# Kernel optimization log

Measured on AMD Instinct MI355X. Metric: run time of the kernel, lower is better.

## Reference

```python
import jax, jax.numpy as jnp
import numpy as np

N, E = 50000, 800000
D_IN, D_HID, D_OUT = 256, 64, 32
LEAKY_SLOPE = 0.2  # PyG GATConv default negative_slope


def _gat(x, src, dst, W, a_src, a_dst, b, n):
    """Single-head PyG-style GATConv: gather -> edge softmax(dst) -> scatter."""
    h = x @ W                                            # [N, C]
    e = jax.nn.leaky_relu((h * a_src).sum(-1)[src] + (h * a_dst).sum(-1)[dst], LEAKY_SLOPE)  # [E]
    m = jax.ops.segment_max(e, dst, num_segments=n)      # per-dst max for stable softmax
    m = jnp.where(jnp.isfinite(m), m, 0.0)               # empty segments -> 0
    p = jnp.exp(e - m[dst])
    s = jax.ops.segment_sum(p, dst, num_segments=n)
    alpha = p / (s[dst] + 1e-16)                         # PyG softmax eps
    out = jax.ops.segment_sum(alpha[:, None] * h[src], dst, num_segments=n) + b
    return out, alpha


def setup_inputs() -> dict:
    key = jax.random.key(0)
    ks = jax.random.split(key, 16)
    g = lambda k, shape, sc: jax.random.normal(k, shape, jnp.float32) * sc
    glorot = lambda fi, fo: (2.0 / (fi + fo)) ** 0.5
    return {
        "x": g(ks[0], (N, D_IN), 1.0),
        "edge_index": jax.random.randint(ks[1], (2, E), 0, N),
        "W1": g(ks[2], (D_IN, D_HID), glorot(D_IN, D_HID)),
        "a1_src": g(ks[3], (D_HID,), 0.1),
        "a1_dst": g(ks[4], (D_HID,), 0.1),
        "b1": jnp.zeros((D_HID,), jnp.float32),
        "W2": g(ks[5], (D_HID, D_OUT), glorot(D_HID, D_OUT)),
        "a2_src": g(ks[6], (D_OUT,), 0.1),
        "a2_dst": g(ks[7], (D_OUT,), 0.1),
        "b2": jnp.zeros((D_OUT,), jnp.float32),
        "W3": g(ks[8], (D_HID, D_OUT), glorot(D_HID, D_OUT)),
        "a3_src": g(ks[9], (D_OUT,), 0.1),
        "a3_dst": g(ks[10], (D_OUT,), 0.1),
        "b3": jnp.zeros((D_OUT,), jnp.float32),
        "Wl": g(ks[11], (D_OUT, D_OUT), glorot(D_OUT, D_OUT)),
        "bl": jnp.zeros((D_OUT,), jnp.float32),
    }


def reference(x, edge_index, W1, a1_src, a1_dst, b1, W2, a2_src, a2_dst, b2,
              W3, a3_src, a3_dst, b3, Wl, bl):
    n = x.shape[0]
    src, dst = edge_index[0], edge_index[1]
    # eval mode: dropout(p=0.6) is identity
    h1, _ = _gat(x, src, dst, W1, a1_src, a1_dst, b1, n)
    h1 = jax.nn.elu(h1)
    mean, alpha = _gat(h1, src, dst, W2, a2_src, a2_dst, b2, n)
    mean = jax.nn.relu(mean)
    # conv_var uses PyG default add_self_loops=True
    loop = jnp.arange(n)
    src3 = jnp.concatenate([src, loop])
    dst3 = jnp.concatenate([dst, loop])
    var, _ = _gat(h1, src3, dst3, W3, a3_src, a3_dst, b3, n)
    mean = mean @ Wl + bl
    return mean, var, alpha
```

## Files before the change

kernel.cpp:

```cpp
#include <hip/hip_runtime.h>
#include <hip/hip_fp16.h>
#include <math.h>

#define N_NODES 50000
#define N_EDGES 800000
#define D_INF   256
#define D_HID   64
#define D_OUTF  32
#define LEAKY   0.2f

#define MT 32
#define KB 16

__device__ __forceinline__ float leaky_relu(float x){ return x >= 0.f ? x : LEAKY * x; }

union H4 { __half2 h[2]; float2 f; };
union H8 { __half2 h[4]; float4 f; };

__device__ __forceinline__ float ldg_f(const float* base, unsigned byteoff){
  return *(const float*)((const char*)base + byteoff);
}

__global__ void k_zero(int* __restrict__ deg){
  int i = blockIdx.x * blockDim.x + threadIdx.x;
  if (i < N_NODES) deg[i] = 0;
}

__global__ void k_deg(const int* __restrict__ dst, int* __restrict__ deg,
                      int* __restrict__ rank){
  int i = blockIdx.x * blockDim.x + threadIdx.x;
  if (i < N_EDGES) rank[i] = atomicAdd(&deg[dst[i]], 1);
}

__global__ __launch_bounds__(256) void k_scan_a(const int* __restrict__ deg, int* __restrict__ bsum){
  __shared__ int ws[4];
  int b = blockIdx.x, t = threadIdx.x, i = b * 256 + t;
  int x = (i < N_NODES) ? deg[i] : 0;
  #pragma unroll
  for (int off = 32; off; off >>= 1) x += __shfl_down(x, off, 64);
  if ((t & 63) == 0) ws[t >> 6] = x;
  __syncthreads();
  if (t == 0) bsum[b] = ws[0] + ws[1] + ws[2] + ws[3];
}

__global__ __launch_bounds__(256) void k_scan_b(int* __restrict__ bsum, int nb,
      const float* __restrict__ W2, const float* __restrict__ W3,
      const float* __restrict__ a2s, const float* __restrict__ a2d,
      const float* __restrict__ a3s, const float* __restrict__ a3d,
      float* __restrict__ prew){
  __shared__ int ws[4];
  int t = threadIdx.x, lane = t & 63, wv = t >> 6;
  int x = (t < nb) ? bsum[t] : 0;
  #pragma unroll
  for (int off = 1; off < 64; off <<= 1){
    int y = __shfl_up(x, off, 64);
    if (lane >= off) x += y;
  }
  if (lane == 63) ws[wv] = x;
  __syncthreads();
  int add = 0;
  for (int w = 0; w < wv; ++w) add += ws[w];
  x += add;
  if (t < nb) bsum[t] = x;

  int vec = t >> 6, k = t & 63;
  const float* W = (vec < 2) ? W2 : W3;
  const float* a = (vec == 0) ? a2s : (vec == 1) ? a2d : (vec == 2) ? a3s : a3d;
  float s = 0.f;
  #pragma unroll 8
  for (int c = 0; c < D_OUTF; ++c) s = fmaf(W[k * D_OUTF + c], a[c], s);
  prew[t] = s;
}

__global__ __launch_bounds__(256) void k_scan_c(const int* __restrict__ deg,
        const int* __restrict__ bsum, int* __restrict__ rowptr){
  __shared__ int ws[4];
  int b = blockIdx.x, t = threadIdx.x, i = b * 256 + t;
  int lane = t & 63, wv = t >> 6;
  int x = (i < N_NODES) ? deg[i] : 0;
  #pragma unroll
  for (int off = 1; off < 64; off <<= 1){
    int y = __shfl_up(x, off, 64);
    if (lane >= off) x += y;
  }
  if (lane == 63) ws[wv] = x;
  __syncthreads();
  int add = (b > 0) ? bsum[b - 1] : 0;
  for (int w = 0; w < wv; ++w) add += ws[w];
  x += add;
  if (i < N_NODES) rowptr[i + 1] = x;
  if (b == 0 && t == 0) rowptr[0] = 0;
}

__global__ void k_fill(const int* __restrict__ src, const int* __restrict__ dst,
                       const int* __restrict__ rowptr, const int* __restrict__ rank,
                       int* __restrict__ srcs){
  int i = blockIdx.x * blockDim.x + threadIdx.x;
  if (i < N_EDGES){
    srcs[rowptr[dst[i]] + rank[i]] = src[i];
  }
}

__global__ __launch_bounds__(256) void k_gemm1(const float* __restrict__ x,
        const float* __restrict__ W1,
        const float* __restrict__ a_src, const float* __restrict__ a_dst,
        __half* __restrict__ h1h, float* __restrict__ es, float* __restrict__ ed){
  __shared__ float xs[2][MT][KB + 4];
  __shared__ float ws[2][KB][D_HID];
  const int tid = threadIdx.x;
  const int tc  = tid & 15;
  const int tr  = tid >> 4;
  const int row0 = blockIdx.x * MT;

  const int lxr = tid >> 2;
  const int lxp = (tid & 3) << 2;
  const int gxrow = row0 + lxr;
  const bool xok = (tid < 128) && (gxrow < N_NODES);
  const float* xbase = x + (size_t)gxrow * D_INF + lxp;
  const int lwr = tid >> 4;
  const int lwp = (tid & 15) << 2;
  const float* wbase = W1 + lwr * D_HID + lwp;

  float4 xv = xok ? *(const float4*)xbase : make_float4(0.f,0.f,0.f,0.f);
  float4 wv = *(const float4*)wbase;
  if (tid < 128) *(float4*)&xs[0][lxr][lxp] = xv;
  *(float4*)&ws[0][lwr][lwp] = wv;
  __syncthreads();

  float acc[2][4] = {};
  int b = 0;
  #pragma unroll 1
  for (int ks = 0; ks < D_INF / KB; ++ks){
    if (ks < D_INF / KB - 1){
      xv = xok ? *(const float4*)(xbase + (ks + 1) * KB) : make_float4(0.f,0.f,0.f,0.f);
      wv = *(const float4*)(wbase + (size_t)(ks + 1) * KB * D_HID);
    }
    #pragma unroll
    for (int k4 = 0; k4 < KB / 4; ++k4){
      float4 xr4[2];
      #pragma unroll
      for (int r = 0; r < 2; ++r)
        xr4[r] = *(float4*)&xs[b][(tr << 1) + r][k4 << 2];
      #pragma unroll
      for (int j = 0; j < 4; ++j){
        float4 w4 = *(float4*)&ws[b][(k4 << 2) + j][tc << 2];
        #pragma unroll
        for (int r = 0; r < 2; ++r){
          float xk = (j == 0) ? xr4[r].x : (j == 1) ? xr4[r].y : (j == 2) ? xr4[r].z : xr4[r].w;
          acc[r][0] = fmaf(xk, w4.x, acc[r][0]);
          acc[r][1] = fmaf(xk, w4.y, acc[r][1]);
          acc[r][2] = fmaf(xk, w4.z, acc[r][2]);
          acc[r][3] = fmaf(xk, w4.w, acc[r][3]);
        }
      }
    }
    if (ks < D_INF / KB - 1){
      if (tid < 128) *(float4*)&xs[b ^ 1][lxr][lxp] = xv;
      *(float4*)&ws[b ^ 1][lwr][lwp] = wv;
    }
    __syncthreads();
    b ^= 1;
  }

  float as0 = a_src[tc << 2], as1 = a_src[(tc << 2) + 1],
        as2 = a_src[(tc << 2) + 2], as3 = a_src[(tc << 2) + 3];
  float ad0 = a_dst[tc << 2], ad1 = a_dst[(tc << 2) + 1],
        ad2 = a_dst[(tc << 2) + 2], ad3 = a_dst[(tc << 2) + 3];
  #pragma unroll
  for (int r = 0; r < 2; ++r){
    int row = row0 + (tr << 1) + r;
    float ps = acc[r][0]*as0 + acc[r][1]*as1 + acc[r][2]*as2 + acc[r][3]*as3;
    float pd = acc[r][0]*ad0 + acc[r][1]*ad1 + acc[r][2]*ad2 + acc[r][3]*ad3;
    #pragma unroll
    for (int off = 1; off < 16; off <<= 1){
      ps += __shfl_xor(ps, off, 64);
      pd += __shfl_xor(pd, off, 64);
    }
    if (row < N_NODES){
      H4 u;
      u.h[0] = __floats2half2_rn(acc[r][0], acc[r][1]);
      u.h[1] = __floats2half2_rn(acc[r][2], acc[r][3]);
      *(float2*)&h1h[(size_t)row * D_HID + (tc << 2)] = u.f;
      if (tc == 0){ es[row] = ps; ed[row] = pd; }
    }
  }
}

__global__ __launch_bounds__(256) void k_agg1(const int* __restrict__ rowptr,
      const int* __restrict__ srcs, const __half* __restrict__ h1,
      const float* __restrict__ es, const float* __restrict__ ed,
      const float* __restrict__ b1, __half* __restrict__ h1act){
  int t = threadIdx.x, lane = t & 63, wv = t >> 6;
  int nh = lane >> 5, sub = lane & 31;
  int slot2 = sub >> 3, cg = sub & 7;
  unsigned coff = cg << 4;

  int node = blockIdx.x * 8 + wv * 2 + nh;
  int beg = rowptr[node], end = rowptr[node + 1];
  int len = end - beg;
  int lenO = __shfl_xor(len, 32, 64);
  int lenmax = len > lenO ? len : lenO;
  int fallback = (len > 0) ? end - 1 : 0;
  float edv = ed[node];
  float4 aL = {0,0,0,0}, aH = {0,0,0,0};
  float ss = 0.f;
  for (int off = 0; off < lenmax; off += 16){
    int sA[4]; float4 vr[4]; float p[4];
    #pragma unroll
    for (int u = 0; u < 4; ++u){
      int idx = beg + off + (u << 2) + slot2;
      sA[u] = srcs[idx < end ? idx : fallback];
    }
    #pragma unroll
    for (int u = 0; u < 4; ++u)
      vr[u] = *(const float4*)((const char*)h1 + ((unsigned)sA[u] << 7) + coff);
    #pragma unroll
    for (int u = 0; u < 4; ++u){
      float e = __expf(leaky_relu(ldg_f(es, (unsigned)sA[u] << 2) + edv));
      p[u] = ((off + (u << 2) + slot2) < len) ? e : 0.f;
    }
    #pragma unroll
    for (int u = 0; u < 4; ++u){
      ss += p[u];
      H8 hh; hh.f = vr[u];
      float2 c0 = __half22float2(hh.h[0]);
      float2 c1 = __half22float2(hh.h[1]);
      float2 c2 = __half22float2(hh.h[2]);
      float2 c3 = __half22float2(hh.h[3]);
      aL.x = fmaf(p[u], c0.x, aL.x); aL.y = fmaf(p[u], c0.y, aL.y);
      aL.z = fmaf(p[u], c1.x, aL.z); aL.w = fmaf(p[u], c1.y, aL.w);
      aH.x = fmaf(p[u], c2.x, aH.x); aH.y = fmaf(p[u], c2.y, aH.y);
      aH.z = fmaf(p[u], c3.x, aH.z); aH.w = fmaf(p[u], c3.y, aH.w);
    }
  }
  #pragma unroll
  for (int off = 8; off <= 16; off <<= 1){
    aL.x += __shfl_xor(aL.x, off, 64); aL.y += __shfl_xor(aL.y, off, 64);
    aL.z += __shfl_xor(aL.z, off, 64); aL.w += __shfl_xor(aL.w, off, 64);
    aH.x += __shfl_xor(aH.x, off, 64); aH.y += __shfl_xor(aH.y, off, 64);
    aH.z += __shfl_xor(aH.z, off, 64); aH.w += __shfl_xor(aH.w, off, 64);
    ss   += __shfl_xor(ss,   off, 64);
  }
  if (slot2 == 0){
    float inv = 1.f / (ss + 1e-16f);
    int ch0 = cg << 3;
    float4 bA = *(const float4*)&b1[ch0];
    float4 bB = *(const float4*)&b1[ch0 + 4];
    float v0 = aL.x * inv + bA.x; v0 = v0 > 0.f ? v0 : expm1f(v0);
    float v1 = aL.y * inv + bA.y; v1 = v1 > 0.f ? v1 : expm1f(v1);
    float v2 = aL.z * inv + bA.z; v2 = v2 > 0.f ? v2 : expm1f(v2);
    float v3 = aL.w * inv + bA.w; v3 = v3 > 0.f ? v3 : expm1f(v3);
    float v4 = aH.x * inv + bB.x; v4 = v4 > 0.f ? v4 : expm1f(v4);
    float v5 = aH.y * inv + bB.y; v5 = v5 > 0.f ? v5 : expm1f(v5);
    float v6 = aH.z * inv + bB.z; v6 = v6 > 0.f ? v6 : expm1f(v6);
    float v7 = aH.w * inv + bB.w; v7 = v7 > 0.f ? v7 : expm1f(v7);
    H8 o;
    o.h[0] = __floats2half2_rn(v0, v1);
    o.h[1] = __floats2half2_rn(v2, v3);
    o.h[2] = __floats2half2_rn(v4, v5);
    o.h[3] = __floats2half2_rn(v6, v7);
    *(float4*)&h1act[(size_t)node * D_HID + ch0] = o.f;
  }
}

__global__ __launch_bounds__(256) void k_gemm23(const __half* __restrict__ h1acth,
        const float* __restrict__ W2, const float* __restrict__ W3,
        const float* __restrict__ prew,
        __half* __restrict__ h23h, float2* __restrict__ es23,
        float2* __restrict__ edinv2, float* __restrict__ ed3){
  __shared__ float hs[64][68];
  __shared__ float wsd[64][64];
  __shared__ float sprew[256];
  const int tid = threadIdx.x;
  const int row0 = blockIdx.x * 64;

  {
    int r = tid >> 2, cg = tid & 3;
    int grow = row0 + r;
    bool ok = grow < N_NODES;
    const float4* hrow = (const float4*)(h1acth + (size_t)grow * D_HID + cg * 16);
    H8 q0, q1;
    q0.f = ok ? hrow[0] : make_float4(0,0,0,0);
    q1.f = ok ? hrow[1] : make_float4(0,0,0,0);
    float* dsth = &hs[r][cg * 16];
    #pragma unroll
    for (int j = 0; j < 4; ++j){
      float2 f = __half22float2(q0.h[j]);
      dsth[j * 2] = f.x; dsth[j * 2 + 1] = f.y;
    }
    #pragma unroll
    for (int j = 0; j < 4; ++j){
      float2 f = __half22float2(q1.h[j]);
      dsth[8 + j * 2] = f.x; dsth[8 + j * 2 + 1] = f.y;
    }
    int k = tid >> 2;
    const float* Wsrc = (cg < 2) ? W2 : W3;
    int cbase = (cg & 1) * 16;
    float4* dstw = (float4*)&wsd[k][cg * 16];
    const float4* srcw = (const float4*)&Wsrc[k * D_OUTF + cbase];
    #pragma unroll
    for (int j = 0; j < 4; ++j) dstw[j] = srcw[j];
    sprew[tid] = prew[tid];
  }
  __syncthreads();

  {
    int r = tid >> 2, q = tid & 3, row = row0 + r;
    float d0 = 0.f, d1 = 0.f, d2 = 0.f, d3 = 0.f;
    #pragma unroll
    for (int k = 0; k < 16; ++k){
      float hval = hs[r][(q << 4) + k];
      d0 = fmaf(hval, sprew[(q << 4) + k], d0);
      d1 = fmaf(hval, sprew[64 + (q << 4) + k], d1);
      d2 = fmaf(hval, sprew[128 + (q << 4) + k], d2);
      d3 = fmaf(hval, sprew[192 + (q << 4) + k], d3);
    }
    #pragma unroll
    for (int off = 1; off < 4; off <<= 1){
      d0 += __shfl_xor(d0, off, 64);
      d1 += __shfl_xor(d1, off, 64);
      d2 += __shfl_xor(d2, off, 64);
      d3 += __shfl_xor(d3, off, 64);
    }
    if (q == 0 && row < N_NODES){
      es23[row] = make_float2(d0, d2);
      edinv2[row].x = d1;
      ed3[row] = d3;
    }
  }

  const int tc = tid & 15, tr = tid >> 4;
  float acc[4][4] = {};
  #pragma unroll
  for (int k4 = 0; k4 < 16; ++k4){
    float4 xr4[4];
    #pragma unroll
    for (int r = 0; r < 4; ++r)
      xr4[r] = *(float4*)&hs[(tr << 2) + r][k4 << 2];
    #pragma unroll
    for (int j = 0; j < 4; ++j){
      float4 w4 = *(float4*)&wsd[(k4 << 2) + j][tc << 2];
      #pragma unroll
      for (int r = 0; r < 4; ++r){
        float xk = (j == 0) ? xr4[r].x : (j == 1) ? xr4[r].y : (j == 2) ? xr4[r].z : xr4[r].w;
        acc[r][0] = fmaf(xk, w4.x, acc[r][0]);
        acc[r][1] = fmaf(xk, w4.y, acc[r][1]);
        acc[r][2] = fmaf(xk, w4.z, acc[r][2]);
        acc[r][3] = fmaf(xk, w4.w, acc[r][3]);
      }
    }
  }
  #pragma unroll
  for (int r = 0; r < 4; ++r){
    int row = row0 + (tr << 2) + r;
    if (row < N_NODES){
      H4 u;
      u.h[0] = __floats2half2_rn(acc[r][0], acc[r][1]);
      u.h[1] = __floats2half2_rn(acc[r][2], acc[r][3]);
      *(float2*)&h23h[(size_t)row * 64 + (tc << 2)] = u.f;
    }
  }
}

__global__ __launch_bounds__(256) void k_agg23(const int* __restrict__ rowptr,
   const int* __restrict__ srcs, const __half* __restrict__ h23,
   const float2* __restrict__ es23, float2* __restrict__ edinv2,
   const float* __restrict__ ed3,
   const float* __restrict__ b2, const float* __restrict__ b3,
   const float* __restrict__ Wlin, const float* __restrict__ blin,
   float* __restrict__ mean_out, float* __restrict__ var_out){
  __shared__ float sWl[D_OUTF * D_OUTF];
  int t = threadIdx.x, lane = t & 63, wv = t >> 6;
  int nh = lane >> 5, sub = lane & 31;
  int slot2 = sub >> 3, cg = sub & 7;
  int layer = cg >> 2;
  unsigned coff = cg << 4;
  for (int idx = t; idx < D_OUTF * D_OUTF; idx += 256) sWl[idx] = Wlin[idx];
  __syncthreads();

  int node = blockIdx.x * 8 + wv * 2 + nh;
  int beg = rowptr[node], end = rowptr[node + 1];
  int len = end - beg;
  int lenO = __shfl_xor(len, 32, 64);
  int lenmax = len > lenO ? len : lenO;
  int fallback = (len > 0) ? end - 1 : 0;
  float edv = layer ? ed3[node] : edinv2[node].x;
  float4 aL = {0,0,0,0}, aH = {0,0,0,0};
  float ss = 0.f;
  for (int off = 0; off < lenmax; off += 16){
    int sA[4]; float4 vr[4]; float p[4];
    #pragma unroll
    for (int u = 0; u < 4; ++u){
      int idx = beg + off + (u << 2) + slot2;
      sA[u] = srcs[idx < end ? idx : fallback];
    }
    #pragma unroll
    for (int u = 0; u < 4; ++u)
      vr[u] = *(const float4*)((const char*)h23 + ((unsigned)sA[u] << 7) + coff);
    #pragma unroll
    for (int u = 0; u < 4; ++u){
      float2 e2 = *(const float2*)((const char*)es23 + ((unsigned)sA[u] << 3));
      float esv = layer ? e2.y : e2.x;
      float e = __expf(leaky_relu(esv + edv));
      p[u] = ((off + (u << 2) + slot2) < len) ? e : 0.f;
    }
    #pragma unroll
    for (int u = 0; u < 4; ++u){
      ss += p[u];
      H8 hh; hh.f = vr[u];
      float2 c0 = __half22float2(hh.h[0]);
      float2 c1 = __half22float2(hh.h[1]);
      float2 c2 = __half22float2(hh.h[2]);
      float2 c3 = __half22float2(hh.h[3]);
      aL.x = fmaf(p[u], c0.x, aL.x); aL.y = fmaf(p[u], c0.y, aL.y);
      aL.z = fmaf(p[u], c1.x, aL.z); aL.w = fmaf(p[u], c1.y, aL.w);
      aH.x = fmaf(p[u], c2.x, aH.x); aH.y = fmaf(p[u], c2.y, aH.y);
      aH.z = fmaf(p[u], c3.x, aH.z); aH.w = fmaf(p[u], c3.y, aH.w);
    }
  }
  #pragma unroll
  for (int off = 8; off <= 16; off <<= 1){
    aL.x += __shfl_xor(aL.x, off, 64); aL.y += __shfl_xor(aL.y, off, 64);
    aL.z += __shfl_xor(aL.z, off, 64); aL.w += __shfl_xor(aL.w, off, 64);
    aH.x += __shfl_xor(aH.x, off, 64); aH.y += __shfl_xor(aH.y, off, 64);
    aH.z += __shfl_xor(aH.z, off, 64); aH.w += __shfl_xor(aH.w, off, 64);
    ss   += __shfl_xor(ss,   off, 64);
  }

  {
    float psr = __expf(leaky_relu(es23[node].y + ed3[node]));
    float psg = layer ? psr : 0.f;
    H8 hh; hh.f = *(const float4*)((const char*)h23 + ((unsigned)node << 7) + coff);
    float2 c0 = __half22float2(hh.h[0]);
    float2 c1 = __half22float2(hh.h[1]);
    float2 c2 = __half22float2(hh.h[2]);
    float2 c3 = __half22float2(hh.h[3]);
    aL.x = fmaf(psg, c0.x, aL.x); aL.y = fmaf(psg, c0.y, aL.y);
    aL.z = fmaf(psg, c1.x, aL.z); aL.w = fmaf(psg, c1.y, aL.w);
    aH.x = fmaf(psg, c2.x, aH.x); aH.y = fmaf(psg, c2.y, aH.y);
    aH.z = fmaf(psg, c3.x, aH.z); aH.w = fmaf(psg, c3.y, aH.w);
    ss += psg;
  }
  float inv = 1.f / (ss + 1e-16f);

  float m0=0,m1=0,m2=0,m3=0,m4=0,m5=0,m6=0,m7=0;
  if (!layer){
    int ch0 = cg << 3;
    float4 bA = *(const float4*)&b2[ch0];
    float4 bB = *(const float4*)&b2[ch0 + 4];
    m0 = aL.x * inv + bA.x; m0 = m0 > 0.f ? m0 : 0.f;
    m1 = aL.y * inv + bA.y; m1 = m1 > 0.f ? m1 : 0.f;
    m2 = aL.z * inv + bA.z; m2 = m2 > 0.f ? m2 : 0.f;
    m3 = aL.w * inv + bA.w; m3 = m3 > 0.f ? m3 : 0.f;
    m4 = aH.x * inv + bB.x; m4 = m4 > 0.f ? m4 : 0.f;
    m5 = aH.y * inv + bB.y; m5 = m5 > 0.f ? m5 : 0.f;
    m6 = aH.z * inv + bB.z; m6 = m6 > 0.f ? m6 : 0.f;
    m7 = aH.w * inv + bB.w; m7 = m7 > 0.f ? m7 : 0.f;
  } else if (slot2 == 0){
    int ch0 = (cg & 3) << 3;
    float4 bA = *(const float4*)&b3[ch0];
    float4 bB = *(const float4*)&b3[ch0 + 4];
    float4 oA = { aL.x * inv + bA.x, aL.y * inv + bA.y, aL.z * inv + bA.z, aL.w * inv + bA.w };
    float4 oB = { aH.x * inv + bB.x, aH.y * inv + bB.y, aH.z * inv + bB.z, aH.w * inv + bB.w };
    *(float4*)&var_out[(size_t)node * D_OUTF + ch0]     = oA;
    *(float4*)&var_out[(size_t)node * D_OUTF + ch0 + 4] = oB;
  }

  {
    int c = sub;
    int lbase = lane & 32;
    float o = blin[c];
    #pragma unroll
    for (int cgs = 0; cgs < 4; ++cgs){
      int sl = lbase | cgs;
      float q0 = __shfl(m0, sl, 64), q1 = __shfl(m1, sl, 64);
      float q2 = __shfl(m2, sl, 64), q3 = __shfl(m3, sl, 64);
      float q4 = __shfl(m4, sl, 64), q5 = __shfl(m5, sl, 64);
      float q6 = __shfl(m6, sl, 64), q7 = __shfl(m7, sl, 64);
      int j0 = cgs << 3;
      o = fmaf(q0, sWl[(j0+0) * D_OUTF + c], o);
      o = fmaf(q1, sWl[(j0+1) * D_OUTF + c], o);
      o = fmaf(q2, sWl[(j0+2) * D_OUTF + c], o);
      o = fmaf(q3, sWl[(j0+3) * D_OUTF + c], o);
      o = fmaf(q4, sWl[(j0+4) * D_OUTF + c], o);
      o = fmaf(q5, sWl[(j0+5) * D_OUTF + c], o);
      o = fmaf(q6, sWl[(j0+6) * D_OUTF + c], o);
      o = fmaf(q7, sWl[(j0+7) * D_OUTF + c], o);
    }
    mean_out[(size_t)node * D_OUTF + c] = o;
  }
  if (sub == 0) edinv2[node].y = inv;
}

__global__ __launch_bounds__(256) void k_alpha(const int* __restrict__ src,
    const int* __restrict__ dst,
    const float2* __restrict__ es23, const float2* __restrict__ edinv2,
    float* __restrict__ alpha_out){
  int e = blockIdx.x * blockDim.x + threadIdx.x;
  if (e < N_EDGES){
    int s = src[e], d = dst[e];
    float2 ei = *(const float2*)((const char*)edinv2 + ((unsigned)d << 3));
    float esv = ((const float2*)((const char*)es23 + ((unsigned)s << 3)))->x;
    alpha_out[e] = __expf(leaky_relu(esv + ei.x)) * ei.y;
  }
}

extern "C" void kernel_launch(void* const* d_in, const int* in_sizes, int n_in,
                              void* d_out, int out_size, void* d_ws, size_t ws_size,
                              hipStream_t stream) {
  const float* x   = (const float*)d_in[0];
  const int*   ei  = (const int*)d_in[1];
  const int*   src = ei;
  const int*   dst = ei + N_EDGES;
  const float* W1  = (const float*)d_in[2];
  const float* a1s = (const float*)d_in[3];
  const float* a1d = (const float*)d_in[4];
  const float* b1  = (const float*)d_in[5];
  const float* W2  = (const float*)d_in[6];
  const float* a2s = (const float*)d_in[7];
  const float* a2d = (const float*)d_in[8];
  const float* b2  = (const float*)d_in[9];
  const float* W3  = (const float*)d_in[10];
  const float* a3s = (const float*)d_in[11];
  const float* a3d = (const float*)d_in[12];
  const float* b3  = (const float*)d_in[13];
  const float* Wl  = (const float*)d_in[14];
  const float* bl  = (const float*)d_in[15];

  float* out       = (float*)d_out;
  float* mean_out  = out;
  float* var_out   = out + (size_t)N_NODES * D_OUTF;
  float* alpha_out = out + 2 * (size_t)N_NODES * D_OUTF;

  const int NSCAN = (N_NODES + 255) / 256;

  int* deg      = (int*)d_ws;
  int* rowptr   = deg + N_NODES;
  int* bsum     = rowptr + (N_NODES + 1);
  int* rank     = bsum + NSCAN;
  int* srcs     = rank + N_EDGES;
  size_t ioff   = (size_t)((srcs + N_EDGES) - (int*)d_ws);
  ioff = (ioff + 3) & ~(size_t)3;
  __half* h1    = (__half*)((int*)d_ws + ioff);
  __half* h1act = h1 + (size_t)N_NODES * 64;
  __half* h23   = h1act + (size_t)N_NODES * 64;
  float* es1    = (float*)(h23 + (size_t)N_NODES * 64);
  float* ed1    = es1 + N_NODES;
  float* ed3    = ed1 + N_NODES;
  float* prew   = ed3 + N_NODES;
  float2* es23  = (float2*)(prew + 256);
  float2* edinv2= es23 + N_NODES;

  k_zero  <<<NSCAN, 256, 0, stream>>>(deg);
  k_deg   <<<(N_EDGES + 255) / 256, 256, 0, stream>>>(dst, deg, rank);
  k_scan_a<<<NSCAN, 256, 0, stream>>>(deg, bsum);
  k_scan_b<<<1, 256, 0, stream>>>(bsum, NSCAN, W2, W3, a2s, a2d, a3s, a3d, prew);
  k_scan_c<<<NSCAN, 256, 0, stream>>>(deg, bsum, rowptr);
  k_fill  <<<(N_EDGES + 255) / 256, 256, 0, stream>>>(src, dst, rowptr, rank, srcs);

  k_gemm1<<<(N_NODES + MT - 1) / MT, 256, 0, stream>>>(x, W1, a1s, a1d, h1, es1, ed1);
  k_agg1 <<<N_NODES / 8, 256, 0, stream>>>(rowptr, srcs, h1, es1, ed1, b1, h1act);
  k_gemm23<<<(N_NODES + 63) / 64, 256, 0, stream>>>(h1act, W2, W3, prew,
                                                    h23, es23, edinv2, ed3);
  k_agg23<<<N_NODES / 8, 256, 0, stream>>>(rowptr, srcs, h23, es23, edinv2, ed3,
                                           b2, b3, Wl, bl, mean_out, var_out);
  k_alpha<<<(N_EDGES + 255) / 256, 256, 0, stream>>>(src, dst, es23, edinv2, alpha_out);
}
```

Measured before the change: 189.9 us.

## Use fp16 MFMA for the first-layer GEMM with W1 staged in LDS

```diff
diff --git a/kernel.cpp b/kernel.cpp
--- a/kernel.cpp
+++ b/kernel.cpp
@@ -9,13 +9,13 @@
 #define D_OUTF  32
 #define LEAKY   0.2f
 
-#define MT 32
-#define KB 16
-
 __device__ __forceinline__ float leaky_relu(float x){ return x >= 0.f ? x : LEAKY * x; }
 
 union H4 { __half2 h[2]; float2 f; };
 union H8 { __half2 h[4]; float4 f; };
+
+typedef __attribute__((ext_vector_type(8))) _Float16 half8;
+typedef __attribute__((ext_vector_type(4))) float f32x4;
 
 __device__ __forceinline__ float ldg_f(const float* base, unsigned byteoff){
   return *(const float*)((const char*)base + byteoff);
@@ -105,83 +105,63 @@
         const float* __restrict__ W1,
         const float* __restrict__ a_src, const float* __restrict__ a_dst,
         __half* __restrict__ h1h, float* __restrict__ es, float* __restrict__ ed){
-  __shared__ float xs[2][MT][KB + 4];
-  __shared__ float ws[2][KB][D_HID];
-  const int tid = threadIdx.x;
-  const int tc  = tid & 15;
-  const int tr  = tid >> 4;
-  const int row0 = blockIdx.x * MT;
-
-  const int lxr = tid >> 2;
-  const int lxp = (tid & 3) << 2;
-  const int gxrow = row0 + lxr;
-  const bool xok = (tid < 128) && (gxrow < N_NODES);
-  const float* xbase = x + (size_t)gxrow * D_INF + lxp;
-  const int lwr = tid >> 4;
-  const int lwp = (tid & 15) << 2;
-  const float* wbase = W1 + lwr * D_HID + lwp;
-
-  float4 xv = xok ? *(const float4*)xbase : make_float4(0.f,0.f,0.f,0.f);
-  float4 wv = *(const float4*)wbase;
-  if (tid < 128) *(float4*)&xs[0][lxr][lxp] = xv;
-  *(float4*)&ws[0][lwr][lwp] = wv;
+  __shared__ _Float16 wlds[64][264];
+  const int tid = threadIdx.x, lane = tid & 63, w = tid >> 6;
+  const int row0 = blockIdx.x * 64 + w * 16;
+
+  for (int idx = tid; idx < 64 * 256; idx += 256){
+    int n = idx & 63, k = idx >> 6;
+    wlds[n][k] = (_Float16)W1[k * 64 + n];
+  }
   __syncthreads();
 
-  float acc[2][4] = {};
-  int b = 0;
-  #pragma unroll 1
-  for (int ks = 0; ks < D_INF / KB; ++ks){
-    if (ks < D_INF / KB - 1){
-      xv = xok ? *(const float4*)(xbase + (ks + 1) * KB) : make_float4(0.f,0.f,0.f,0.f);
-      wv = *(const float4*)(wbase + (size_t)(ks + 1) * KB * D_HID);
-    }
-    #pragma unroll
-    for (int k4 = 0; k4 < KB / 4; ++k4){
-      float4 xr4[2];
-      #pragma unroll
-      for (int r = 0; r < 2; ++r)
-        xr4[r] = *(float4*)&xs[b][(tr << 1) + r][k4 << 2];
-      #pragma unroll
-      for (int j = 0; j < 4; ++j){
-        float4 w4 = *(float4*)&ws[b][(k4 << 2) + j][tc << 2];
-        #pragma unroll
-        for (int r = 0; r < 2; ++r){
-          float xk = (j == 0) ? xr4[r].x : (j == 1) ? xr4[r].y : (j == 2) ? xr4[r].z : xr4[r].w;
-          acc[r][0] = fmaf(xk, w4.x, acc[r][0]);
-          acc[r][1] = fmaf(xk, w4.y, acc[r][1]);
-          acc[r][2] = fmaf(xk, w4.z, acc[r][2]);
-          acc[r][3] = fmaf(xk, w4.w, acc[r][3]);
-        }
-      }
-    }
-    if (ks < D_INF / KB - 1){
-      if (tid < 128) *(float4*)&xs[b ^ 1][lxr][lxp] = xv;
-      *(float4*)&ws[b ^ 1][lwr][lwp] = wv;
-    }
-    __syncthreads();
-    b ^= 1;
-  }
-
-  float as0 = a_src[tc << 2], as1 = a_src[(tc << 2) + 1],
-        as2 = a_src[(tc << 2) + 2], as3 = a_src[(tc << 2) + 3];
-  float ad0 = a_dst[tc << 2], ad1 = a_dst[(tc << 2) + 1],
-        ad2 = a_dst[(tc << 2) + 2], ad3 = a_dst[(tc << 2) + 3];
-  #pragma unroll
-  for (int r = 0; r < 2; ++r){
-    int row = row0 + (tr << 1) + r;
-    float ps = acc[r][0]*as0 + acc[r][1]*as1 + acc[r][2]*as2 + acc[r][3]*as3;
-    float pd = acc[r][0]*ad0 + acc[r][1]*ad1 + acc[r][2]*ad2 + acc[r][3]*ad3;
-    #pragma unroll
-    for (int off = 1; off < 16; off <<= 1){
-      ps += __shfl_xor(ps, off, 64);
-      pd += __shfl_xor(pd, off, 64);
-    }
-    if (row < N_NODES){
-      H4 u;
-      u.h[0] = __floats2half2_rn(acc[r][0], acc[r][1]);
-      u.h[1] = __floats2half2_rn(acc[r][2], acc[r][3]);
-      *(float2*)&h1h[(size_t)row * D_HID + (tc << 2)] = u.f;
-      if (tc == 0){ es[row] = ps; ed[row] = pd; }
+  int arow = row0 + (lane & 15);
+  if (arow >= N_NODES) arow = N_NODES - 1;
+  const float* xrow = x + (size_t)arow * D_INF;
+  const int klane = (lane >> 4) * 8;
+
+  f32x4 acc[4] = {{0,0,0,0},{0,0,0,0},{0,0,0,0},{0,0,0,0}};
+  #pragma unroll
+  for (int ks = 0; ks < 8; ++ks){
+    float4 xa = *(const float4*)(xrow + ks * 32 + klane);
+    float4 xb = *(const float4*)(xrow + ks * 32 + klane + 4);
+    half8 a;
+    a[0] = (_Float16)xa.x; a[1] = (_Float16)xa.y; a[2] = (_Float16)xa.z; a[3] = (_Float16)xa.w;
+    a[4] = (_Float16)xb.x; a[5] = (_Float16)xb.y; a[6] = (_Float16)xb.z; a[7] = (_Float16)xb.w;
+    #pragma unroll
+    for (int ct = 0; ct < 4; ++ct){
+      half8 b = *(const half8*)&wlds[ct * 16 + (lane & 15)][ks * 32 + klane];
+      acc[ct] = __builtin_amdgcn_mfma_f32_16x16x32_f16(a, b, acc[ct], 0, 0, 0);
+    }
+  }
+
+  float ps[4] = {0,0,0,0}, pd[4] = {0,0,0,0};
+  #pragma unroll
+  for (int ct = 0; ct < 4; ++ct){
+    int col = ct * 16 + (lane & 15);
+    float as = a_src[col], ad = a_dst[col];
+    #pragma unroll
+    for (int r = 0; r < 4; ++r){
+      int row = row0 + (lane >> 4) * 4 + r;
+      if (row < N_NODES)
+        h1h[(size_t)row * D_HID + col] = __float2half_rn(acc[ct][r]);
+      ps[r] = fmaf(acc[ct][r], as, ps[r]);
+      pd[r] = fmaf(acc[ct][r], ad, pd[r]);
+    }
+  }
+  #pragma unroll
+  for (int off = 1; off < 16; off <<= 1){
+    #pragma unroll
+    for (int r = 0; r < 4; ++r){
+      ps[r] += __shfl_xor(ps[r], off, 64);
+      pd[r] += __shfl_xor(pd[r], off, 64);
+    }
+  }
+  if ((lane & 15) == 0){
+    #pragma unroll
+    for (int r = 0; r < 4; ++r){
+      int row = row0 + (lane >> 4) * 4 + r;
+      if (row < N_NODES){ es[row] = ps[r]; ed[row] = pd[r]; }
     }
   }
 }
@@ -558,7 +538,7 @@
   k_scan_c<<<NSCAN, 256, 0, stream>>>(deg, bsum, rowptr);
   k_fill  <<<(N_EDGES + 255) / 256, 256, 0, stream>>>(src, dst, rowptr, rank, srcs);
 
-  k_gemm1<<<(N_NODES + MT - 1) / MT, 256, 0, stream>>>(x, W1, a1s, a1d, h1, es1, ed1);
+  k_gemm1<<<(N_NODES + 63) / 64, 256, 0, stream>>>(x, W1, a1s, a1d, h1, es1, ed1);
   k_agg1 <<<N_NODES / 8, 256, 0, stream>>>(rowptr, srcs, h1, es1, ed1, b1, h1act);
   k_gemm23<<<(N_NODES + 63) / 64, 256, 0, stream>>>(h1act, W2, W3, prew,
                                                     h23, es23, edinv2, ed3);
```

Result: faster. 173.8 us (-8.5%).
